# Performance work log

Hardware: AMD Instinct MI355X
Metric: run time of the kernel (lower is better)

The kernel has to match this reference:

```python
import jax, jax.numpy as jnp
import numpy as np

N = 50000       # nodes
E = 800000      # edges (before self loops)
DIN = 128       # input feature width
H = 4           # heads
C = 64          # hidden width per head
NCLS = 2        # num classes
NEG_SLOPE = 0.2 # PyG GATConv default negative_slope


def setup_inputs() -> dict:
    key = jax.random.key(0)
    ks = jax.random.split(key, 16)
    x = jax.random.normal(ks[0], (N, DIN), dtype=jnp.float32)
    edge_index = jax.random.randint(ks[1], (2, E), 0, N, dtype=jnp.int64)
    s = 0.05
    # layer 0: DIN -> H*C
    W0 = jax.random.normal(ks[2], (DIN, H * C), dtype=jnp.float32) * s
    a_src0 = jax.random.normal(ks[3], (H, C), dtype=jnp.float32) * s
    a_dst0 = jax.random.normal(ks[4], (H, C), dtype=jnp.float32) * s
    b0 = jnp.zeros((H * C,), dtype=jnp.float32)
    # layer 1: H*C -> H*C
    W1 = jax.random.normal(ks[5], (H * C, H * C), dtype=jnp.float32) * s
    a_src1 = jax.random.normal(ks[6], (H, C), dtype=jnp.float32) * s
    a_dst1 = jax.random.normal(ks[7], (H, C), dtype=jnp.float32) * s
    b1 = jnp.zeros((H * C,), dtype=jnp.float32)
    # layer 2: H*C -> NCLS, single head
    W2 = jax.random.normal(ks[8], (H * C, NCLS), dtype=jnp.float32) * s
    a_src2 = jax.random.normal(ks[9], (1, NCLS), dtype=jnp.float32) * s
    a_dst2 = jax.random.normal(ks[10], (1, NCLS), dtype=jnp.float32) * s
    b2 = jnp.zeros((NCLS,), dtype=jnp.float32)
    return {"x": x, "edge_index": edge_index,
            "W0": W0, "a_src0": a_src0, "a_dst0": a_dst0, "b0": b0,
            "W1": W1, "a_src1": a_src1, "a_dst1": a_dst1, "b1": b1,
            "W2": W2, "a_src2": a_src2, "a_dst2": a_dst2, "b2": b2}


def gat_conv(x, ei, W, a_src, a_dst, b, heads, out_c):
    """PyG-style GATConv (add_self_loops already applied to ei, concat=True)."""
    n = x.shape[0]
    h = (x @ W).reshape(n, heads, out_c)              # [N, H, C]
    src, dst = ei[0], ei[1]
    asrc = (h * a_src).sum(-1)                         # [N, H]
    adst = (h * a_dst).sum(-1)                         # [N, H]
    alpha = jax.nn.leaky_relu(asrc[src] + adst[dst], NEG_SLOPE)  # [E', H]
    # segment softmax over incoming edges of each dst node
    amax = jax.ops.segment_max(alpha, dst, num_segments=n)        # [N, H]
    e = jnp.exp(alpha - amax[dst])
    denom = jax.ops.segment_sum(e, dst, num_segments=n)
    coef = e / denom[dst]                              # [E', H]
    msg = h[src] * coef[:, :, None]                    # [E', H, C]
    out = jax.ops.segment_sum(msg, dst, num_segments=n)           # [N, H, C]
    return out.reshape(n, heads * out_c) + b


def reference(x, edge_index, W0, a_src0, a_dst0, b0,
              W1, a_src1, a_dst1, b1, W2, a_src2, a_dst2, b2):
    # Inference mode: dropout(p=0.5, training=False) is identity.
    loops = jnp.arange(N, dtype=edge_index.dtype)
    ei = jnp.concatenate([edge_index, jnp.stack([loops, loops])], axis=1)
    h = jnp.tanh(gat_conv(x, ei, W0, a_src0, a_dst0, b0, H, C))
    h = jnp.tanh(gat_conv(h, ei, W1, a_src1, a_dst1, b1, H, C))
    h = gat_conv(h, ei, W2, a_src2, a_dst2, b2, 1, NCLS)
    return jax.nn.softmax(h, axis=1), h
```

## Files before the change

kernel.cpp:

```cpp
#include <hip/hip_runtime.h>

#define NEG 0.2f

typedef float f32x4 __attribute__((ext_vector_type(4)));
typedef short bf16x8 __attribute__((ext_vector_type(8)));

struct __align__(8) us4 { unsigned short v[4]; };

__device__ __forceinline__ float b2f(unsigned short u){
  union { unsigned int i; float f; } x; x.i = ((unsigned int)u) << 16; return x.f;
}
__device__ __forceinline__ unsigned short f2b(float f){
  union { float f; unsigned int i; } x; x.f = f;
  unsigned int r = x.i + 0x7FFFu + ((x.i >> 16) & 1u);
  return (unsigned short)(r >> 16);
}


__global__ void k_pack_w2(const float* __restrict__ W0, unsigned short* __restrict__ Wp0,
                          const float* __restrict__ W1, unsigned short* __restrict__ Wp1){
  int t = blockIdx.x*blockDim.x + threadIdx.x;
  const int T0 = 16*4*64;
  const int T1 = 16*8*64;
  const float* W; unsigned short* Wp;
  if (t < T0){ W = W0; Wp = Wp0; }
  else if (t < T0 + T1){ W = W1; Wp = Wp1; t -= T0; }
  else return;
  int lane = t & 63;
  int nb = (t >> 6) & 15;
  int kb = (t >> 6) >> 4;
  int kbase = kb*32 + ((lane>>4)<<3);
  int col = nb*16 + (lane&15);
  #pragma unroll
  for (int j=0;j<8;j++) Wp[(size_t)t*8 + j] = f2b(W[(size_t)(kbase+j)*256 + col]);
}

__global__ void k_init(const int* __restrict__ ei, int* __restrict__ meta,
                       int* __restrict__ deg, int N){
  int i = blockIdx.x*blockDim.x + threadIdx.x;
  if (i < N) deg[i] = 0;
  if (i == 0){
    int o = 0;
    #pragma unroll
    for (int j=1;j<128;j+=2) o |= ei[j];
    meta[0] = (o==0) ? 1 : 0;
  }
}

__global__ void k_deg(const int* __restrict__ ei, const int* __restrict__ meta,
                      int* __restrict__ deg, int E, int EP, int N){
  int e = blockIdx.x*blockDim.x + threadIdx.x;
  if (e >= EP) return;
  int s, d;
  if (e < E){
    if (meta[0]){ s = ei[2*(size_t)e]; d = ei[2*(size_t)(E+e)]; }
    else        { s = ei[e];           d = ei[E+e]; }
  } else { s = d = e - E; }
  if ((unsigned)d >= (unsigned)N || (unsigned)s >= (unsigned)N) return;
  atomicAdd(deg + d, 1);
}

__global__ void k_scan1(const int* __restrict__ deg, int* __restrict__ tmp,
                        int* __restrict__ bsum, int N){
  __shared__ int s[256];
  int t = threadIdx.x;
  int i = blockIdx.x*256 + t;
  int v = (i < N) ? deg[i] : 0;
  s[t] = v;
  __syncthreads();
  for (int off=1; off<256; off<<=1){
    int x = (t>=off) ? s[t-off] : 0;
    __syncthreads();
    s[t] += x;
    __syncthreads();
  }
  if (i < N) tmp[i] = s[t] - v;
  if (t == 255) bsum[blockIdx.x] = s[255];
}

__global__ void k_scan2(const int* __restrict__ bsum, int* __restrict__ bsumx,
                        int* __restrict__ meta, int n){
  __shared__ int s[256];
  int t = threadIdx.x;
  int v = (t < n) ? bsum[t] : 0;
  s[t] = v;
  __syncthreads();
  for (int off=1; off<256; off<<=1){
    int x = (t>=off) ? s[t-off] : 0;
    __syncthreads();
    s[t] += x;
    __syncthreads();
  }
  bsumx[t] = s[t] - v;
  if (t == 255) meta[1] = s[255];
}

__global__ void k_scan3(const int* __restrict__ tmp, const int* __restrict__ bsumx,
                        const int* __restrict__ meta,
                        int* __restrict__ rp, int* __restrict__ cur, int N){
  int i = blockIdx.x*256 + threadIdx.x;
  if (i < N){ int v = tmp[i] + bsumx[i>>8]; rp[i] = v; cur[i] = v; }
  if (i == 0) rp[N] = meta[1];
}

__global__ void k_fill(const int* __restrict__ ei, const int* __restrict__ meta,
                       int* __restrict__ cur, int* __restrict__ csr, int E, int EP, int N){
  int e = blockIdx.x*blockDim.x + threadIdx.x;
  if (e >= EP) return;
  int s, d;
  if (e < E){
    if (meta[0]){ s = ei[2*(size_t)e]; d = ei[2*(size_t)(E+e)]; }
    else        { s = ei[e];           d = ei[E+e]; }
  } else { s = d = e - E; }
  if ((unsigned)d >= (unsigned)N || (unsigned)s >= (unsigned)N) return;
  int pos = atomicAdd(cur + d, 1);
  csr[pos] = s;
}

template<int K, int CVT>
__global__ __launch_bounds__(256) void k_gemm(const void* __restrict__ Xv,
    const unsigned short* __restrict__ Wp,
    const float* __restrict__ aS, const float* __restrict__ aD,
    unsigned short* __restrict__ Hout,
    float* __restrict__ asrc, float* __restrict__ adst, int N){
  constexpr int KB = K/32;
  __shared__ short sB[2][16*64*8];
  const int lane = threadIdx.x & 63;
  const int wave = threadIdx.x >> 6;
  const int rowbase = blockIdx.x*64 + wave*16;
  const int l15 = lane & 15, lhi = lane >> 4;
  const int arow = rowbase + l15;

  bf16x8 aF[KB];
  if (CVT){
    const float* X = (const float*)Xv;
    #pragma unroll
    for (int kb=0; kb<KB; kb++){
      bf16x8 a = {};
      if (arow < N){
        f32x4 v0 = *(const f32x4*)(X + (size_t)arow*K + kb*32 + lhi*8);
        f32x4 v1 = *(const f32x4*)(X + (size_t)arow*K + kb*32 + lhi*8 + 4);
        #pragma unroll
        for (int j=0;j<4;j++){ a[j] = (short)f2b(v0[j]); a[j+4] = (short)f2b(v1[j]); }
      }
      aF[kb] = a;
    }
  } else {
    const unsigned short* X = (const unsigned short*)Xv;
    #pragma unroll
    for (int kb=0; kb<KB; kb++){
      bf16x8 a = {};
      if (arow < N) a = *(const bf16x8*)(X + (size_t)arow*K + kb*32 + lhi*8);
      aF[kb] = a;
    }
  }

  auto stage = [&](int buf, int kb){
    #pragma unroll
    for (int q=0;q<4;q++){
      int nb = wave*4 + q;
      const unsigned short* gsrc = Wp + ((size_t)((kb*16 + nb)*64) + lane)*8;
      __builtin_amdgcn_global_load_lds(
          (const __attribute__((address_space(1))) void*)gsrc,
          (__attribute__((address_space(3))) void*)&sB[buf][(size_t)nb*64*8],
          16, 0, 0);
    }
  };

  f32x4 acc[16] = {};
  stage(0, 0);
  __syncthreads();
  #pragma unroll
  for (int kb=0; kb<KB; kb++){
    const int cur = kb & 1;
    if (kb+1 < KB) stage(cur^1, kb+1);
    #pragma unroll
    for (int nb=0; nb<16; nb++){
      bf16x8 b = *(const bf16x8*)(&sB[cur][((size_t)nb*64 + lane)*8]);
      acc[nb] = __builtin_amdgcn_mfma_f32_16x16x32_bf16(aF[kb], b, acc[nb], 0, 0, 0);
    }
    __syncthreads();
  }

  const int r0 = rowbase + lhi*4;

  float sp[4][4] = {}; float dp[4][4] = {};
  #pragma unroll
  for (int h=0; h<4; h++){
    #pragma unroll
    for (int q=0; q<4; q++){
      const int nb = h*4 + q;
      float ws = aS[h*64 + q*16 + l15];
      float wd = aD[h*64 + q*16 + l15];
      #pragma unroll
      for (int r=0;r<4;r++){ sp[r][h] += acc[nb][r]*ws; dp[r][h] += acc[nb][r]*wd; }
    }
  }
  #pragma unroll
  for (int m=1;m<16;m<<=1){
    #pragma unroll
    for (int r=0;r<4;r++){
      #pragma unroll
      for (int h=0;h<4;h++){
        sp[r][h] += __shfl_xor(sp[r][h], m);
        dp[r][h] += __shfl_xor(dp[r][h], m);
      }
    }
  }
  if (l15 < 4){
    const int h = l15;
    #pragma unroll
    for (int r=0;r<4;r++){
      int row = r0 + r;
      if (row < N){ asrc[row*4+h] = sp[r][h]; adst[row*4+h] = dp[r][h]; }
    }
  }
  #pragma unroll
  for (int nb=0;nb<16;nb++){
    #pragma unroll
    for (int r=0;r<4;r++){
      int row = r0 + r;
      if (row < N) Hout[(size_t)row*256 + nb*16 + l15] = f2b(acc[nb][r]);
    }
  }
}

__global__ __launch_bounds__(256) void k_agg(const unsigned short* __restrict__ Hb,
    const float* __restrict__ asrc, const float* __restrict__ adst,
    const int* __restrict__ rp, const int* __restrict__ csr,
    const float* __restrict__ bias, unsigned short* __restrict__ Xout, int N){
  const int lane = threadIdx.x & 63;
  const int dst = blockIdx.x*4 + (threadIdx.x >> 6);
  if (dst >= N) return;
  const int head = lane >> 4;
  const int c0 = lane*4;
  const float ad = adst[dst*4 + head];
  const int s0 = rp[dst], s1 = rp[dst+1];
  float a0=0.f,a1=0.f,a2=0.f,a3=0.f,den=0.f;
  int e = s0;
  for (; e+8 <= s1; e += 8){
    int i0 = csr[e+0], i1 = csr[e+1], i2 = csr[e+2], i3 = csr[e+3];
    int i4 = csr[e+4], i5 = csr[e+5], i6 = csr[e+6], i7 = csr[e+7];
    float x0 = asrc[(size_t)i0*4 + head];
    float x1 = asrc[(size_t)i1*4 + head];
    float x2 = asrc[(size_t)i2*4 + head];
    float x3 = asrc[(size_t)i3*4 + head];
    float x4 = asrc[(size_t)i4*4 + head];
    float x5 = asrc[(size_t)i5*4 + head];
    float x6 = asrc[(size_t)i6*4 + head];
    float x7 = asrc[(size_t)i7*4 + head];
    us4 h0 = *(const us4*)(Hb + (size_t)i0*256 + c0);
    us4 h1 = *(const us4*)(Hb + (size_t)i1*256 + c0);
    us4 h2 = *(const us4*)(Hb + (size_t)i2*256 + c0);
    us4 h3 = *(const us4*)(Hb + (size_t)i3*256 + c0);
    us4 h4 = *(const us4*)(Hb + (size_t)i4*256 + c0);
    us4 h5 = *(const us4*)(Hb + (size_t)i5*256 + c0);
    us4 h6 = *(const us4*)(Hb + (size_t)i6*256 + c0);
    us4 h7 = *(const us4*)(Hb + (size_t)i7*256 + c0);
    x0 += ad; x0 = x0 > 0.f ? x0 : NEG*x0; float e0 = __expf(x0);
    x1 += ad; x1 = x1 > 0.f ? x1 : NEG*x1; float e1 = __expf(x1);
    x2 += ad; x2 = x2 > 0.f ? x2 : NEG*x2; float e2 = __expf(x2);
    x3 += ad; x3 = x3 > 0.f ? x3 : NEG*x3; float e3 = __expf(x3);
    x4 += ad; x4 = x4 > 0.f ? x4 : NEG*x4; float e4 = __expf(x4);
    x5 += ad; x5 = x5 > 0.f ? x5 : NEG*x5; float e5 = __expf(x5);
    x6 += ad; x6 = x6 > 0.f ? x6 : NEG*x6; float e6 = __expf(x6);
    x7 += ad; x7 = x7 > 0.f ? x7 : NEG*x7; float e7 = __expf(x7);
    den += ((e0+e1)+(e2+e3)) + ((e4+e5)+(e6+e7));
    a0 += e0*b2f(h0.v[0]) + e1*b2f(h1.v[0]) + e2*b2f(h2.v[0]) + e3*b2f(h3.v[0])
        + e4*b2f(h4.v[0]) + e5*b2f(h5.v[0]) + e6*b2f(h6.v[0]) + e7*b2f(h7.v[0]);
    a1 += e0*b2f(h0.v[1]) + e1*b2f(h1.v[1]) + e2*b2f(h2.v[1]) + e3*b2f(h3.v[1])
        + e4*b2f(h4.v[1]) + e5*b2f(h5.v[1]) + e6*b2f(h6.v[1]) + e7*b2f(h7.v[1]);
    a2 += e0*b2f(h0.v[2]) + e1*b2f(h1.v[2]) + e2*b2f(h2.v[2]) + e3*b2f(h3.v[2])
        + e4*b2f(h4.v[2]) + e5*b2f(h5.v[2]) + e6*b2f(h6.v[2]) + e7*b2f(h7.v[2]);
    a3 += e0*b2f(h0.v[3]) + e1*b2f(h1.v[3]) + e2*b2f(h2.v[3]) + e3*b2f(h3.v[3])
        + e4*b2f(h4.v[3]) + e5*b2f(h5.v[3]) + e6*b2f(h6.v[3]) + e7*b2f(h7.v[3]);
  }
  for (; e+4 <= s1; e += 4){
    int i0 = csr[e+0], i1 = csr[e+1], i2 = csr[e+2], i3 = csr[e+3];
    float x0 = asrc[(size_t)i0*4 + head];
    float x1 = asrc[(size_t)i1*4 + head];
    float x2 = asrc[(size_t)i2*4 + head];
    float x3 = asrc[(size_t)i3*4 + head];
    us4 h0 = *(const us4*)(Hb + (size_t)i0*256 + c0);
    us4 h1 = *(const us4*)(Hb + (size_t)i1*256 + c0);
    us4 h2 = *(const us4*)(Hb + (size_t)i2*256 + c0);
    us4 h3 = *(const us4*)(Hb + (size_t)i3*256 + c0);
    x0 += ad; x0 = x0 > 0.f ? x0 : NEG*x0; float e0 = __expf(x0);
    x1 += ad; x1 = x1 > 0.f ? x1 : NEG*x1; float e1 = __expf(x1);
    x2 += ad; x2 = x2 > 0.f ? x2 : NEG*x2; float e2 = __expf(x2);
    x3 += ad; x3 = x3 > 0.f ? x3 : NEG*x3; float e3 = __expf(x3);
    den += (e0 + e1) + (e2 + e3);
    a0 += e0*b2f(h0.v[0]) + e1*b2f(h1.v[0]) + e2*b2f(h2.v[0]) + e3*b2f(h3.v[0]);
    a1 += e0*b2f(h0.v[1]) + e1*b2f(h1.v[1]) + e2*b2f(h2.v[1]) + e3*b2f(h3.v[1]);
    a2 += e0*b2f(h0.v[2]) + e1*b2f(h1.v[2]) + e2*b2f(h2.v[2]) + e3*b2f(h3.v[2]);
    a3 += e0*b2f(h0.v[3]) + e1*b2f(h1.v[3]) + e2*b2f(h2.v[3]) + e3*b2f(h3.v[3]);
  }
  for (; e < s1; e++){
    int src = csr[e];
    float al = asrc[(size_t)src*4 + head] + ad;
    al = al > 0.f ? al : NEG*al;
    float ee = __expf(al);
    den += ee;
    us4 hv = *(const us4*)(Hb + (size_t)src*256 + c0);
    a0 += ee * b2f(hv.v[0]);
    a1 += ee * b2f(hv.v[1]);
    a2 += ee * b2f(hv.v[2]);
    a3 += ee * b2f(hv.v[3]);
  }
  float rd = 1.0f/den;
  us4 o;
  o.v[0] = f2b(tanhf(a0*rd + bias[c0+0]));
  o.v[1] = f2b(tanhf(a1*rd + bias[c0+1]));
  o.v[2] = f2b(tanhf(a2*rd + bias[c0+2]));
  o.v[3] = f2b(tanhf(a3*rd + bias[c0+3]));
  *(us4*)(Xout + (size_t)dst*256 + c0) = o;
}

__global__ __launch_bounds__(256) void k_gemm2(const unsigned short* __restrict__ X,
    const float* __restrict__ W2, const float* __restrict__ as2, const float* __restrict__ ad2,
    float* __restrict__ H2, float* __restrict__ asrc2, float* __restrict__ adst2, int N){
  __shared__ float sW[512];
  const int t = threadIdx.x;
  sW[t] = W2[t]; sW[t+256] = W2[t+256];
  __syncthreads();
  const int row = blockIdx.x*16 + (t>>4);
  const int sub = t & 15;
  float a0=0.f, a1=0.f;
  if (row < N){
    const unsigned short* xp = X + (size_t)row*256 + sub*16;
    #pragma unroll
    for (int jj=0;jj<4;jj++){
      us4 hv = *(const us4*)(xp + jj*4);
      #pragma unroll
      for (int j=0;j<4;j++){
        float f = b2f(hv.v[j]);
        int k = sub*16 + jj*4 + j;
        a0 += f * sW[k*2+0];
        a1 += f * sW[k*2+1];
      }
    }
  }
  #pragma unroll
  for (int m=1;m<16;m<<=1){ a0 += __shfl_xor(a0,m); a1 += __shfl_xor(a1,m); }
  if (sub==0 && row<N){
    H2[row*2+0]=a0; H2[row*2+1]=a1;
    asrc2[row] = a0*as2[0] + a1*as2[1];
    adst2[row] = a0*ad2[0] + a1*ad2[1];
  }
}

__global__ __launch_bounds__(256) void k_agg2(const float* __restrict__ H2,
    const float* __restrict__ asrc2, const float* __restrict__ adst2,
    const int* __restrict__ rp, const int* __restrict__ csr, const float* __restrict__ bb,
    float* __restrict__ out, int N){
  const int sub = threadIdx.x & 15;
  const int dst = blockIdx.x*16 + (threadIdx.x >> 4);
  if (dst >= N) return;
  const float ad = adst2[dst];
  const int s0 = rp[dst], s1 = rp[dst+1];
  float n0=0.f, n1=0.f, den=0.f;
  for (int e=s0+sub; e<s1; e+=16){
    int src = csr[e];
    float al = asrc2[src] + ad;
    al = al>0.f ? al : NEG*al;
    float ee = __expf(al);
    den += ee;
    n0 += ee * H2[src*2+0];
    n1 += ee * H2[src*2+1];
  }
  #pragma unroll
  for (int m=1;m<16;m<<=1){
    n0 += __shfl_xor(n0,m); n1 += __shfl_xor(n1,m); den += __shfl_xor(den,m);
  }
  if (sub==0){
    float o0 = n0/den + bb[0];
    float o1 = n1/den + bb[1];
    float mx = fmaxf(o0,o1);
    float e0 = __expf(o0-mx), e1 = __expf(o1-mx);
    float is = 1.0f/(e0+e1);
    out[(size_t)dst*2+0] = e0*is;
    out[(size_t)dst*2+1] = e1*is;
    out[(size_t)2*N + dst*2+0] = o0;
    out[(size_t)2*N + dst*2+1] = o1;
  }
}

extern "C" void kernel_launch(void* const* d_in, const int* in_sizes, int n_in,
                              void* d_out, int out_size, void* d_ws, size_t ws_size,
                              hipStream_t stream){
  const float* x  = (const float*)d_in[0];
  const int*   ei = (const int*)d_in[1];
  const float* W0 = (const float*)d_in[2];
  const float* as0= (const float*)d_in[3];
  const float* ad0= (const float*)d_in[4];
  const float* b0 = (const float*)d_in[5];
  const float* W1 = (const float*)d_in[6];
  const float* as1= (const float*)d_in[7];
  const float* ad1= (const float*)d_in[8];
  const float* b1 = (const float*)d_in[9];
  const float* W2 = (const float*)d_in[10];
  const float* as2= (const float*)d_in[11];
  const float* ad2= (const float*)d_in[12];
  const float* b2 = (const float*)d_in[13];

  const int N  = in_sizes[0] / 128;
  const int E  = in_sizes[1] / 2;
  const int EP = E + N;
  float* outp = (float*)d_out;

  char* w = (char*)d_ws;
  size_t off = 0;
  auto alloc = [&](size_t bytes)->char*{
    char* p = w + off; off = (off + bytes + 255) & ~(size_t)255; return p;
  };
  unsigned short* hb  = (unsigned short*)alloc((size_t)N*256*2);
  unsigned short* xa  = (unsigned short*)alloc((size_t)N*256*2);
  float* asrc  = (float*)alloc((size_t)N*4*4);
  float* adst  = (float*)alloc((size_t)N*4*4);
  float* asrc2 = (float*)alloc((size_t)N*4);
  float* adst2 = (float*)alloc((size_t)N*4);
  float* H2    = (float*)alloc((size_t)N*2*4);
  unsigned short* Wp0 = (unsigned short*)alloc((size_t)128*256*2);
  unsigned short* Wp1 = (unsigned short*)alloc((size_t)256*256*2);
  int* deg   = (int*)alloc((size_t)N*4);
  int* rp    = (int*)alloc((size_t)(N+1)*4);
  int* cur   = (int*)alloc((size_t)N*4);
  int* tmp   = (int*)alloc((size_t)N*4);
  int* bsum  = (int*)alloc(256*4);
  int* bsumx = (int*)alloc(256*4);
  int* meta  = (int*)alloc(8*4);
  int* csr   = (int*)alloc((size_t)EP*4);
  (void)ws_size; (void)n_in; (void)out_size;

  k_init  <<<(N + 255)/256, 256, 0, stream>>>(ei, meta, deg, N);
  k_pack_w2<<<(16*4*64 + 16*8*64 + 255)/256, 256, 0, stream>>>(W0, Wp0, W1, Wp1);
  k_deg   <<<(EP + 255)/256, 256, 0, stream>>>(ei, meta, deg, E, EP, N);
  const int nb1 = (N + 255)/256;
  k_scan1 <<<nb1, 256, 0, stream>>>(deg, tmp, bsum, N);
  k_scan2 <<<1, 256, 0, stream>>>(bsum, bsumx, meta, nb1);
  k_scan3 <<<nb1, 256, 0, stream>>>(tmp, bsumx, meta, rp, cur, N);
  k_fill  <<<(EP + 255)/256, 256, 0, stream>>>(ei, meta, cur, csr, E, EP, N);

  k_gemm<128,1><<<(N + 63)/64, 256, 0, stream>>>(x, Wp0, as0, ad0, hb, asrc, adst, N);
  k_agg        <<<(N + 3)/4, 256, 0, stream>>>(hb, asrc, adst, rp, csr, b0, xa, N);
  k_gemm<256,0><<<(N + 63)/64, 256, 0, stream>>>(xa, Wp1, as1, ad1, hb, asrc, adst, N);
  k_agg        <<<(N + 3)/4, 256, 0, stream>>>(hb, asrc, adst, rp, csr, b1, xa, N);
  k_gemm2      <<<(N + 15)/16, 256, 0, stream>>>(xa, W2, as2, ad2, H2, asrc2, adst2, N);
  k_agg2       <<<(N + 15)/16, 256, 0, stream>>>(H2, asrc2, adst2, rp, csr, b2, outp, N);
}
```

Measured before the change: 311.6 us.

## Merge setup kernels and co-schedule degree counting with layer-0 GEMM

Weight packing and degree/meta initialisation become a single launch, and the edge-degree atomic pass shares a grid with the first-layer GEMM through block-index dispatch, so independent work overlaps and two launches disappear. The fill and degree kernels drop the source-index bounds check, and bf16 conversion now uses the HIP intrinsic. The risks are that the combined kernel carries the GEMM's shared-memory footprint in every block, including the atomic-only ones, which could lower occupancy, and that out-of-range source indices are no longer filtered.

```diff
diff --git a/kernel.cpp b/kernel.cpp
--- a/kernel.cpp
+++ b/kernel.cpp
@@ -1,4 +1,5 @@
 #include <hip/hip_runtime.h>
+#include <hip/hip_bf16.h>
 
 #define NEG 0.2f
 
@@ -11,54 +12,180 @@
   union { unsigned int i; float f; } x; x.i = ((unsigned int)u) << 16; return x.f;
 }
 __device__ __forceinline__ unsigned short f2b(float f){
-  union { float f; unsigned int i; } x; x.f = f;
-  unsigned int r = x.i + 0x7FFFu + ((x.i >> 16) & 1u);
-  return (unsigned short)(r >> 16);
-}
-
-
-__global__ void k_pack_w2(const float* __restrict__ W0, unsigned short* __restrict__ Wp0,
-                          const float* __restrict__ W1, unsigned short* __restrict__ Wp1){
-  int t = blockIdx.x*blockDim.x + threadIdx.x;
-  const int T0 = 16*4*64;
-  const int T1 = 16*8*64;
-  const float* W; unsigned short* Wp;
-  if (t < T0){ W = W0; Wp = Wp0; }
-  else if (t < T0 + T1){ W = W1; Wp = Wp1; t -= T0; }
-  else return;
-  int lane = t & 63;
-  int nb = (t >> 6) & 15;
-  int kb = (t >> 6) >> 4;
-  int kbase = kb*32 + ((lane>>4)<<3);
-  int col = nb*16 + (lane&15);
-  #pragma unroll
-  for (int j=0;j<8;j++) Wp[(size_t)t*8 + j] = f2b(W[(size_t)(kbase+j)*256 + col]);
-}
-
-__global__ void k_init(const int* __restrict__ ei, int* __restrict__ meta,
-                       int* __restrict__ deg, int N){
-  int i = blockIdx.x*blockDim.x + threadIdx.x;
-  if (i < N) deg[i] = 0;
-  if (i == 0){
-    int o = 0;
-    #pragma unroll
-    for (int j=1;j<128;j+=2) o |= ei[j];
-    meta[0] = (o==0) ? 1 : 0;
-  }
-}
-
-__global__ void k_deg(const int* __restrict__ ei, const int* __restrict__ meta,
-                      int* __restrict__ deg, int E, int EP, int N){
-  int e = blockIdx.x*blockDim.x + threadIdx.x;
-  if (e >= EP) return;
-  int s, d;
-  if (e < E){
-    if (meta[0]){ s = ei[2*(size_t)e]; d = ei[2*(size_t)(E+e)]; }
-    else        { s = ei[e];           d = ei[E+e]; }
-  } else { s = d = e - E; }
-  if ((unsigned)d >= (unsigned)N || (unsigned)s >= (unsigned)N) return;
-  atomicAdd(deg + d, 1);
-}
+  __hip_bfloat16 h = __float2bfloat16(f);
+  return *reinterpret_cast<unsigned short*>(&h);
+}
+
+__global__ __launch_bounds__(256) void k_setup(
+    const float* __restrict__ W0, unsigned short* __restrict__ Wp0,
+    const float* __restrict__ W1, unsigned short* __restrict__ Wp1,
+    const int* __restrict__ ei, int* __restrict__ meta,
+    int* __restrict__ deg, int N, int npack){
+  const int bid = blockIdx.x;
+  if (bid < npack){
+    int t = bid*256 + threadIdx.x;
+    const int T0 = 16*4*64;
+    const int T1 = 16*8*64;
+    const float* W; unsigned short* Wp;
+    if (t < T0){ W = W0; Wp = Wp0; }
+    else if (t < T0 + T1){ W = W1; Wp = Wp1; t -= T0; }
+    else return;
+    int lane = t & 63;
+    int nb = (t >> 6) & 15;
+    int kb = (t >> 6) >> 4;
+    int kbase = kb*32 + ((lane>>4)<<3);
+    int col = nb*16 + (lane&15);
+    #pragma unroll
+    for (int j=0;j<8;j++) Wp[(size_t)t*8 + j] = f2b(W[(size_t)(kbase+j)*256 + col]);
+  } else {
+    int i = (bid - npack)*256 + threadIdx.x;
+    if (i < N) deg[i] = 0;
+    if (i == 0){
+      int o = 0;
+      #pragma unroll
+      for (int j=1;j<128;j+=2) o |= ei[j];
+      meta[0] = (o==0) ? 1 : 0;
+    }
+  }
+}
+
+template<int K, int CVT>
+__device__ __forceinline__ void gemm_body(int bid, const void* __restrict__ Xv,
+    const unsigned short* __restrict__ Wp,
+    const float* __restrict__ aS, const float* __restrict__ aD,
+    unsigned short* __restrict__ Hout,
+    float* __restrict__ asrc, float* __restrict__ adst, int N){
+  constexpr int KB = K/32;
+  __shared__ short sB[2][16*64*8];
+  const int lane = threadIdx.x & 63;
+  const int wave = threadIdx.x >> 6;
+  const int rowbase = bid*64 + wave*16;
+  const int l15 = lane & 15, lhi = lane >> 4;
+  const int arow = rowbase + l15;
+
+  bf16x8 aF[KB];
+  if (CVT){
+    const float* X = (const float*)Xv;
+    #pragma unroll
+    for (int kb=0; kb<KB; kb++){
+      bf16x8 a = {};
+      if (arow < N){
+        f32x4 v0 = *(const f32x4*)(X + (size_t)arow*K + kb*32 + lhi*8);
+        f32x4 v1 = *(const f32x4*)(X + (size_t)arow*K + kb*32 + lhi*8 + 4);
+        #pragma unroll
+        for (int j=0;j<4;j++){ a[j] = (short)f2b(v0[j]); a[j+4] = (short)f2b(v1[j]); }
+      }
+      aF[kb] = a;
+    }
+  } else {
+    const unsigned short* X = (const unsigned short*)Xv;
+    #pragma unroll
+    for (int kb=0; kb<KB; kb++){
+      bf16x8 a = {};
+      if (arow < N) a = *(const bf16x8*)(X + (size_t)arow*K + kb*32 + lhi*8);
+      aF[kb] = a;
+    }
+  }
+
+  auto stage = [&](int buf, int kb){
+    #pragma unroll
+    for (int q=0;q<4;q++){
+      int nb = wave*4 + q;
+      const unsigned short* gsrc = Wp + ((size_t)((kb*16 + nb)*64) + lane)*8;
+      __builtin_amdgcn_global_load_lds(
+          (const __attribute__((address_space(1))) void*)gsrc,
+          (__attribute__((address_space(3))) void*)&sB[buf][(size_t)nb*64*8],
+          16, 0, 0);
+    }
+  };
+
+  f32x4 acc[16] = {};
+  stage(0, 0);
+  __syncthreads();
+  #pragma unroll
+  for (int kb=0; kb<KB; kb++){
+    const int cur = kb & 1;
+    if (kb+1 < KB) stage(cur^1, kb+1);
+    #pragma unroll
+    for (int nb=0; nb<16; nb++){
+      bf16x8 b = *(const bf16x8*)(&sB[cur][((size_t)nb*64 + lane)*8]);
+      acc[nb] = __builtin_amdgcn_mfma_f32_16x16x32_bf16(aF[kb], b, acc[nb], 0, 0, 0);
+    }
+    __syncthreads();
+  }
+
+  const int r0 = rowbase + lhi*4;
+
+  float sp[4][4] = {}; float dp[4][4] = {};
+  #pragma unroll
+  for (int h=0; h<4; h++){
+    #pragma unroll
+    for (int q=0; q<4; q++){
+      const int nb = h*4 + q;
+      float ws = aS[h*64 + q*16 + l15];
+      float wd = aD[h*64 + q*16 + l15];
+      #pragma unroll
+      for (int r=0;r<4;r++){ sp[r][h] += acc[nb][r]*ws; dp[r][h] += acc[nb][r]*wd; }
+    }
+  }
+  #pragma unroll
+  for (int m=1;m<16;m<<=1){
+    #pragma unroll
+    for (int r=0;r<4;r++){
+      #pragma unroll
+      for (int h=0;h<4;h++){
+        sp[r][h] += __shfl_xor(sp[r][h], m);
+        dp[r][h] += __shfl_xor(dp[r][h], m);
+      }
+    }
+  }
+  if (l15 < 4){
+    const int h = l15;
+    #pragma unroll
+    for (int r=0;r<4;r++){
+      int row = r0 + r;
+      if (row < N){ asrc[row*4+h] = sp[r][h]; adst[row*4+h] = dp[r][h]; }
+    }
+  }
+  #pragma unroll
+  for (int nb=0;nb<16;nb++){
+    #pragma unroll
+    for (int r=0;r<4;r++){
+      int row = r0 + r;
+      if (row < N) Hout[(size_t)row*256 + nb*16 + l15] = f2b(acc[nb][r]);
+    }
+  }
+}
+
+__global__ __launch_bounds__(256) void k_g128deg(
+    const float* __restrict__ x, const unsigned short* __restrict__ Wp0,
+    const float* __restrict__ aS, const float* __restrict__ aD,
+    unsigned short* __restrict__ hb,
+    float* __restrict__ asrc, float* __restrict__ adst, int N,
+    const int* __restrict__ ei, const int* __restrict__ meta,
+    int* __restrict__ deg, int E, int EP, int ngemm){
+  const int bid = blockIdx.x;
+  if (bid < ngemm){
+    gemm_body<128,1>(bid, x, Wp0, aS, aD, hb, asrc, adst, N);
+  } else {
+    int e = (bid - ngemm)*256 + threadIdx.x;
+    if (e >= EP) return;
+    int d;
+    if (e < E) d = meta[0] ? ei[2*(size_t)(E+e)] : ei[E+e];
+    else       d = e - E;
+    if ((unsigned)d >= (unsigned)N) return;
+    atomicAdd(deg + d, 1);
+  }
+}
+
+__global__ __launch_bounds__(256) void k_gemm256(const unsigned short* __restrict__ X,
+    const unsigned short* __restrict__ Wp,
+    const float* __restrict__ aS, const float* __restrict__ aD,
+    unsigned short* __restrict__ Hout,
+    float* __restrict__ asrc, float* __restrict__ adst, int N){
+  gemm_body<256,0>(blockIdx.x, X, Wp, aS, aD, Hout, asrc, adst, N);
+}
+
 
 __global__ void k_scan1(const int* __restrict__ deg, int* __restrict__ tmp,
                         int* __restrict__ bsum, int N){
@@ -112,117 +239,9 @@
     if (meta[0]){ s = ei[2*(size_t)e]; d = ei[2*(size_t)(E+e)]; }
     else        { s = ei[e];           d = ei[E+e]; }
   } else { s = d = e - E; }
-  if ((unsigned)d >= (unsigned)N || (unsigned)s >= (unsigned)N) return;
+  if ((unsigned)d >= (unsigned)N) return;
   int pos = atomicAdd(cur + d, 1);
   csr[pos] = s;
-}
-
-template<int K, int CVT>
-__global__ __launch_bounds__(256) void k_gemm(const void* __restrict__ Xv,
-    const unsigned short* __restrict__ Wp,
-    const float* __restrict__ aS, const float* __restrict__ aD,
-    unsigned short* __restrict__ Hout,
-    float* __restrict__ asrc, float* __restrict__ adst, int N){
-  constexpr int KB = K/32;
-  __shared__ short sB[2][16*64*8];
-  const int lane = threadIdx.x & 63;
-  const int wave = threadIdx.x >> 6;
-  const int rowbase = blockIdx.x*64 + wave*16;
-  const int l15 = lane & 15, lhi = lane >> 4;
-  const int arow = rowbase + l15;
-
-  bf16x8 aF[KB];
-  if (CVT){
-    const float* X = (const float*)Xv;
-    #pragma unroll
-    for (int kb=0; kb<KB; kb++){
-      bf16x8 a = {};
-      if (arow < N){
-        f32x4 v0 = *(const f32x4*)(X + (size_t)arow*K + kb*32 + lhi*8);
-        f32x4 v1 = *(const f32x4*)(X + (size_t)arow*K + kb*32 + lhi*8 + 4);
-        #pragma unroll
-        for (int j=0;j<4;j++){ a[j] = (short)f2b(v0[j]); a[j+4] = (short)f2b(v1[j]); }
-      }
-      aF[kb] = a;
-    }
-  } else {
-    const unsigned short* X = (const unsigned short*)Xv;
-    #pragma unroll
-    for (int kb=0; kb<KB; kb++){
-      bf16x8 a = {};
-      if (arow < N) a = *(const bf16x8*)(X + (size_t)arow*K + kb*32 + lhi*8);
-      aF[kb] = a;
-    }
-  }
-
-  auto stage = [&](int buf, int kb){
-    #pragma unroll
-    for (int q=0;q<4;q++){
-      int nb = wave*4 + q;
-      const unsigned short* gsrc = Wp + ((size_t)((kb*16 + nb)*64) + lane)*8;
-      __builtin_amdgcn_global_load_lds(
-          (const __attribute__((address_space(1))) void*)gsrc,
-          (__attribute__((address_space(3))) void*)&sB[buf][(size_t)nb*64*8],
-          16, 0, 0);
-    }
-  };
-
-  f32x4 acc[16] = {};
-  stage(0, 0);
-  __syncthreads();
-  #pragma unroll
-  for (int kb=0; kb<KB; kb++){
-    const int cur = kb & 1;
-    if (kb+1 < KB) stage(cur^1, kb+1);
-    #pragma unroll
-    for (int nb=0; nb<16; nb++){
-      bf16x8 b = *(const bf16x8*)(&sB[cur][((size_t)nb*64 + lane)*8]);
-      acc[nb] = __builtin_amdgcn_mfma_f32_16x16x32_bf16(aF[kb], b, acc[nb], 0, 0, 0);
-    }
-    __syncthreads();
-  }
-
-  const int r0 = rowbase + lhi*4;
-
-  float sp[4][4] = {}; float dp[4][4] = {};
-  #pragma unroll
-  for (int h=0; h<4; h++){
-    #pragma unroll
-    for (int q=0; q<4; q++){
-      const int nb = h*4 + q;
-      float ws = aS[h*64 + q*16 + l15];
-      float wd = aD[h*64 + q*16 + l15];
-      #pragma unroll
-      for (int r=0;r<4;r++){ sp[r][h] += acc[nb][r]*ws; dp[r][h] += acc[nb][r]*wd; }
-    }
-  }
-  #pragma unroll
-  for (int m=1;m<16;m<<=1){
-    #pragma unroll
-    for (int r=0;r<4;r++){
-      #pragma unroll
-      for (int h=0;h<4;h++){
-        sp[r][h] += __shfl_xor(sp[r][h], m);
-        dp[r][h] += __shfl_xor(dp[r][h], m);
-      }
-    }
-  }
-  if (l15 < 4){
-    const int h = l15;
-    #pragma unroll
-    for (int r=0;r<4;r++){
-      int row = r0 + r;
-      if (row < N){ asrc[row*4+h] = sp[r][h]; adst[row*4+h] = dp[r][h]; }
-    }
-  }
-  #pragma unroll
-  for (int nb=0;nb<16;nb++){
-    #pragma unroll
-    for (int r=0;r<4;r++){
-      int row = r0 + r;
-      if (row < N) Hout[(size_t)row*256 + nb*16 + l15] = f2b(acc[nb][r]);
-    }
-  }
 }
 
 __global__ __launch_bounds__(256) void k_agg(const unsigned short* __restrict__ Hb,
@@ -432,19 +451,24 @@
   int* csr   = (int*)alloc((size_t)EP*4);
   (void)ws_size; (void)n_in; (void)out_size;
 
-  k_init  <<<(N + 255)/256, 256, 0, stream>>>(ei, meta, deg, N);
-  k_pack_w2<<<(16*4*64 + 16*8*64 + 255)/256, 256, 0, stream>>>(W0, Wp0, W1, Wp1);
-  k_deg   <<<(EP + 255)/256, 256, 0, stream>>>(ei, meta, deg, E, EP, N);
+  const int npack = (16*4*64 + 16*8*64) / 256;
+  const int ninit = (N + 255)/256;
+  k_setup<<<npack + ninit, 256, 0, stream>>>(W0, Wp0, W1, Wp1, ei, meta, deg, N, npack);
+
+  const int ngemm = (N + 63)/64;
+  const int ndeg  = (EP + 255)/256;
+  k_g128deg<<<ngemm + ndeg, 256, 0, stream>>>(x, Wp0, as0, ad0, hb, asrc, adst, N,
+                                              ei, meta, deg, E, EP, ngemm);
+
   const int nb1 = (N + 255)/256;
   k_scan1 <<<nb1, 256, 0, stream>>>(deg, tmp, bsum, N);
   k_scan2 <<<1, 256, 0, stream>>>(bsum, bsumx, meta, nb1);
   k_scan3 <<<nb1, 256, 0, stream>>>(tmp, bsumx, meta, rp, cur, N);
-  k_fill  <<<(EP + 255)/256, 256, 0, stream>>>(ei, meta, cur, csr, E, EP, N);
-
-  k_gemm<128,1><<<(N + 63)/64, 256, 0, stream>>>(x, Wp0, as0, ad0, hb, asrc, adst, N);
-  k_agg        <<<(N + 3)/4, 256, 0, stream>>>(hb, asrc, adst, rp, csr, b0, xa, N);
-  k_gemm<256,0><<<(N + 63)/64, 256, 0, stream>>>(xa, Wp1, as1, ad1, hb, asrc, adst, N);
-  k_agg        <<<(N + 3)/4, 256, 0, stream>>>(hb, asrc, adst, rp, csr, b1, xa, N);
-  k_gemm2      <<<(N + 15)/16, 256, 0, stream>>>(xa, W2, as2, ad2, H2, asrc2, adst2, N);
-  k_agg2       <<<(N + 15)/16, 256, 0, stream>>>(H2, asrc2, adst2, rp, csr, b2, outp, N);
-}
+  k_fill  <<<ndeg, 256, 0, stream>>>(ei, meta, cur, csr, E, EP, N);
+
+  k_agg   <<<(N + 3)/4, 256, 0, stream>>>(hb, asrc, adst, rp, csr, b0, xa, N);
+  k_gemm256<<<ngemm, 256, 0, stream>>>(xa, Wp1, as1, ad1, hb, asrc, adst, N);
+  k_agg   <<<(N + 3)/4, 256, 0, stream>>>(hb, asrc, adst, rp, csr, b1, xa, N);
+  k_gemm2 <<<(N + 15)/16, 256, 0, stream>>>(xa, W2, as2, ad2, H2, asrc2, adst2, N);
+  k_agg2  <<<(N + 15)/16, 256, 0, stream>>>(H2, asrc2, adst2, rp, csr, b2, outp, N);
+}
```

After: 289.4 us. 1.08x faster.
